# Optimization experiments

Measured on AMD Instinct MI355X. Metric: run time of the kernel, lower is better.

## Reference

```python
import jax, jax.numpy as jnp
import numpy as np

D_HEAD = 64

def setup_inputs() -> dict:
    key = jax.random.key(0)
    kq, kk, kv, kc = jax.random.split(key, 4)
    B, H, T, D = 2, 16, 2048, D_HEAD
    Q = jax.random.normal(kq, (B, H, T, D), dtype=jnp.float32)
    K = jax.random.normal(kk, (B, H, T, D), dtype=jnp.float32)
    V = jax.random.normal(kv, (B, H, T, D), dtype=jnp.float32)
    # causal mask: True = attend
    mask = jnp.tril(jnp.ones((T, T), dtype=jnp.bool_))
    curvature = jax.random.normal(kc, (H, D, D), dtype=jnp.float32) * 0.02
    return {"Q": Q, "K": K, "V": V, "mask": mask, "curvature": curvature}

def reference(Q, K, V, mask, curvature):
    scale = 1.0 / np.sqrt(Q.shape[-1]).astype(np.float32)
    # per-head learned rotation of Q
    Q_rot = jnp.einsum('bhtd,hde->bhte', Q, curvature)
    scores = jnp.einsum('bhtd,bhsd->bhts', Q_rot, K) * scale  # [B,H,T,T]
    scores = jnp.where(mask[None, None, :, :], scores, -jnp.inf)
    attn = jax.nn.softmax(scores, axis=-1)
    out = jnp.einsum('bhts,bhsd->bhtd', attn, V)
    return out
```

## Files before the change

kernel.cpp:

```cpp
#include <hip/hip_runtime.h>


typedef __attribute__((ext_vector_type(8))) short short8;
typedef __attribute__((ext_vector_type(8))) unsigned short ushort8;
typedef __attribute__((ext_vector_type(4))) float f32x4;
typedef __attribute__((ext_vector_type(2))) _Float16 half2v;
typedef __attribute__((ext_vector_type(4))) _Float16 half4;
typedef __attribute__((ext_vector_type(8))) _Float16 half8;

constexpr int Tc = 2048;
constexpr int Dc = 64;
constexpr size_t REGION = (size_t)32 * Tc * Dc;

__device__ inline unsigned short f2bf(float f) {
    union { float f; unsigned u; } x; x.f = f;
    return (unsigned short)((x.u + 0x7fffu + ((x.u >> 16) & 1u)) >> 16);
}

__device__ inline half2v pkrtz(float a, float b) {
    return __builtin_bit_cast(half2v, __builtin_amdgcn_cvt_pkrtz(a, b));
}

#define MFMA_BF16_K32(a, b, c) __builtin_amdgcn_mfma_f32_16x16x32_bf16((a), (b), (c), 0, 0, 0)
#define MFMA_F16_K16(a, b, c)  __builtin_amdgcn_mfma_f32_16x16x16f16((a), (b), (c), 0, 0, 0)

__global__ __launch_bounds__(256, 1)
void holo_cfrag(const float* __restrict__ Cp, unsigned short* __restrict__ cfrag_g)
{
    const int t = threadIdx.x, lane = t & 63, eb = t >> 6;
    const int l15 = lane & 15, quad = lane >> 4;
    const int h = blockIdx.x;
    const float* Cg = Cp + (size_t)h * Dc * Dc;
    #pragma unroll
    for (int half = 0; half < 2; ++half) {
        short8 b;
        #pragma unroll
        for (int jj = 0; jj < 8; ++jj) {
            const int d = half * 32 + quad * 8 + jj;
            b[jj] = (short)f2bf(Cg[d * Dc + eb * 16 + l15]);
        }
        *(short8*)(&cfrag_g[(((size_t)h * 4 + eb) * 2 + half) * 512 + lane * 8]) = b;
    }
}

__global__ __launch_bounds__(256, 4)
void holo_prep8(const float* __restrict__ Qp, const float* __restrict__ Kp,
                const float* __restrict__ Vp,
                const unsigned short* __restrict__ cfrag_g,
                unsigned short* __restrict__ qfrag_g,
                unsigned short* __restrict__ kfrag_g,
                _Float16* __restrict__ vfrag_g)
{
    __shared__ unsigned short kt[64 * 72];
    __shared__ unsigned short qt[64 * 72];
    __shared__ _Float16      vt[64 * 72];
    __shared__ unsigned short pf[64 * 72];

    const int t = threadIdx.x, lane = t & 63, w = t >> 6;
    const int l15 = lane & 15, quad = lane >> 4, wb = w * 16;
    const int n = blockIdx.x, bh = n >> 5, st = n & 31, h = bh & 15;
    const int s0 = st * 64;

    const float* Qg = Qp + ((size_t)bh * Tc + s0) * Dc;
    const float* Kg = Kp + ((size_t)bh * Tc + s0) * Dc;
    const float* Vg = Vp + ((size_t)bh * Tc + s0) * Dc;

    #pragma unroll
    for (int kk = 0; kk < 4; ++kk) {
        const int flat = kk * 1024 + t * 4;
        const int r = flat >> 6, d0 = flat & 63;
        float4 kv = *(const float4*)(&Kg[flat]);
        ushort4 kp; kp.x = f2bf(kv.x); kp.y = f2bf(kv.y); kp.z = f2bf(kv.z); kp.w = f2bf(kv.w);
        *(ushort4*)(&kt[r * 72 + d0]) = kp;
        float4 qv = *(const float4*)(&Qg[flat]);
        ushort4 qp; qp.x = f2bf(qv.x); qp.y = f2bf(qv.y); qp.z = f2bf(qv.z); qp.w = f2bf(qv.w);
        *(ushort4*)(&qt[r * 72 + d0]) = qp;
        float4 vv = *(const float4*)(&Vg[flat]);
        half4 vp;
        vp[0] = (_Float16)vv.x; vp[1] = (_Float16)vv.y;
        vp[2] = (_Float16)vv.z; vp[3] = (_Float16)vv.w;
        *(half4*)(&vt[r * 72 + d0]) = vp;
    }
    __syncthreads();

    {
        const int row = wb + l15;
        ushort8 p0 = *(const ushort8*)(&kt[row * 72 + quad * 8]);
        ushort8 p1 = *(const ushort8*)(&kt[row * 72 + 32 + quad * 8]);
        unsigned short* kdst = kfrag_g + (((size_t)(bh * 32 + st) * 4 + w) * 64 + lane) * 16;
        *(ushort8*)(kdst) = p0;
        *(ushort8*)(kdst + 8) = p1;
    }

    {
        half8 v0, v1;
        #pragma unroll
        for (int dn = 0; dn < 2; ++dn)
            #pragma unroll
            for (int i = 0; i < 4; ++i)
                v0[dn * 4 + i] = vt[(wb + quad * 4 + i) * 72 + dn * 16 + l15];
        #pragma unroll
        for (int dn = 0; dn < 2; ++dn)
            #pragma unroll
            for (int i = 0; i < 4; ++i)
                v1[dn * 4 + i] = vt[(wb + quad * 4 + i) * 72 + (dn + 2) * 16 + l15];
        _Float16* vdst = vfrag_g + (((size_t)(bh * 32 + st) * 4 + w) * 64 + lane) * 16;
        *(half8*)(vdst) = v0;
        *(half8*)(vdst + 8) = v1;
    }

    {
        short8 a0 = *(const short8*)(&qt[(wb + l15) * 72 + quad * 8]);
        short8 a1 = *(const short8*)(&qt[(wb + l15) * 72 + 32 + quad * 8]);
        #pragma unroll
        for (int eb = 0; eb < 4; ++eb) {
            short8 b0 = *(const short8*)(&cfrag_g[(((size_t)h * 4 + eb) * 2 + 0) * 512 + lane * 8]);
            short8 b1 = *(const short8*)(&cfrag_g[(((size_t)h * 4 + eb) * 2 + 1) * 512 + lane * 8]);
            f32x4 c = {0.f, 0.f, 0.f, 0.f};
            c = MFMA_BF16_K32(a0, b0, c);
            c = MFMA_BF16_K32(a1, b1, c);
            #pragma unroll
            for (int i = 0; i < 4; ++i)
                pf[(wb + quad * 4 + i) * 72 + eb * 16 + l15] = f2bf(c[i] * 0.18033688f);
        }
        __threadfence_block();
        short8 fa0 = *(const short8*)(&pf[(wb + l15) * 72 + quad * 8]);
        short8 fa1 = *(const short8*)(&pf[(wb + l15) * 72 + 32 + quad * 8]);
        const size_t strip = (size_t)bh * 128 + st * 4 + w;
        *(short8*)(&qfrag_g[strip * 1024 + lane * 8]) = fa0;
        *(short8*)(&qfrag_g[strip * 1024 + 512 + lane * 8]) = fa1;
    }
}

__global__ __launch_bounds__(256, 2)
void holo_attn10(const unsigned short* __restrict__ qfrag_g,
                 const unsigned short* __restrict__ kfrag_g,
                 const _Float16* __restrict__ vfrag_g,
                 float* __restrict__ Op)
{
    __shared__ float lds_o[2][2][16][68];
    __shared__ float lds_l[2][2][16];

    const int t = threadIdx.x, lane = t & 63, wid = t >> 6;
    const int l15 = lane & 15, quad = lane >> 4;
    const int hv  = wid & 1;
    const int par = wid >> 1;

    const int id = blockIdx.x;
    const int xcd = id & 7, sseq = id >> 3;
    const int qi = 31 - (sseq >> 2);
    const int bh = xcd * 4 + (sseq & 3);
    const int q0 = qi * 64;

    short8 qa0[2], qa1[2];
    #pragma unroll
    for (int s2 = 0; s2 < 2; ++s2) {
        const size_t strip = (size_t)bh * 128 + qi * 4 + (2 * hv + s2);
        qa0[s2] = *(const short8*)(&qfrag_g[strip * 1024 + lane * 8]);
        qa1[s2] = *(const short8*)(&qfrag_g[strip * 1024 + 512 + lane * 8]);
    }

    const unsigned short* kbase = kfrag_g + (size_t)bh * 32 * 4 * 1024;
    const _Float16*       vbase = vfrag_g + (size_t)bh * 32 * 4 * 1024;

    f32x4 o[2][4];
    #pragma unroll
    for (int s2 = 0; s2 < 2; ++s2)
        #pragma unroll
        for (int dn = 0; dn < 4; ++dn) o[s2][dn] = f32x4{0.f, 0.f, 0.f, 0.f};
    float l2[2] = {0.f, 0.f};

    const int rowgA = q0 + (2 * hv) * 16 + l15;
    const int rowgB = rowgA + 16;

    short8 kf0[4], kf1[4];
    half8 vlo[4], vhi[4];
    #pragma unroll
    for (int tn = 0; tn < 4; ++tn) {
        const unsigned short* kfb = kbase + (size_t)par * 4096 + ((size_t)tn * 64 + lane) * 16;
        kf0[tn] = *(const short8*)(kfb);
        kf1[tn] = *(const short8*)(kfb + 8);
        const _Float16* vfb = vbase + (size_t)par * 4096 + ((size_t)tn * 64 + lane) * 16;
        vlo[tn] = *(const half8*)(vfb);
        vhi[tn] = *(const half8*)(vfb + 8);
    }

    for (int j = par; j <= qi; j += 2) {
        f32x4 stA[4], stB[4];
        #pragma unroll
        for (int tn = 0; tn < 4; ++tn) {
            f32x4 cA = {0.f, 0.f, 0.f, 0.f};
            cA = MFMA_BF16_K32(kf0[tn], qa0[0], cA);
            cA = MFMA_BF16_K32(kf1[tn], qa1[0], cA);
            stA[tn] = cA;
            f32x4 cB = {0.f, 0.f, 0.f, 0.f};
            cB = MFMA_BF16_K32(kf0[tn], qa0[1], cB);
            cB = MFMA_BF16_K32(kf1[tn], qa1[1], cB);
            stB[tn] = cB;
        }

        const int jn = (j + 2 <= qi) ? j + 2 : j;
        #pragma unroll
        for (int tn = 0; tn < 4; ++tn) {
            const unsigned short* kfb = kbase + (size_t)jn * 4096 + ((size_t)tn * 64 + lane) * 16;
            kf0[tn] = *(const short8*)(kfb);
            kf1[tn] = *(const short8*)(kfb + 8);
        }

        half4 paA[4], paB[4];
        #pragma unroll
        for (int tn = 0; tn < 4; ++tn) {
            float pA[4], pB[4];
            #pragma unroll
            for (int i = 0; i < 4; ++i) {
                float svA = stA[tn][i], svB = stB[tn][i];
                if (j == qi) {
                    const int colg = j * 64 + tn * 16 + quad * 4 + i;
                    if (colg > rowgA) svA = -1e30f;
                    if (colg > rowgB) svB = -1e30f;
                }
                pA[i] = __builtin_amdgcn_exp2f(svA);
                pB[i] = __builtin_amdgcn_exp2f(svB);
                l2[0] += pA[i];
                l2[1] += pB[i];
            }
            half2v loA = pkrtz(pA[0], pA[1]), hiA = pkrtz(pA[2], pA[3]);
            paA[tn] = __builtin_shufflevector(loA, hiA, 0, 1, 2, 3);
            half2v loB = pkrtz(pB[0], pB[1]), hiB = pkrtz(pB[2], pB[3]);
            paB[tn] = __builtin_shufflevector(loB, hiB, 0, 1, 2, 3);
        }

        #pragma unroll
        for (int tn = 0; tn < 4; ++tn) {
            half4 vf0 = __builtin_shufflevector(vlo[tn], vlo[tn], 0, 1, 2, 3);
            half4 vf1 = __builtin_shufflevector(vlo[tn], vlo[tn], 4, 5, 6, 7);
            half4 vf2 = __builtin_shufflevector(vhi[tn], vhi[tn], 0, 1, 2, 3);
            half4 vf3 = __builtin_shufflevector(vhi[tn], vhi[tn], 4, 5, 6, 7);
            o[0][0] = MFMA_F16_K16(vf0, paA[tn], o[0][0]);
            o[0][1] = MFMA_F16_K16(vf1, paA[tn], o[0][1]);
            o[0][2] = MFMA_F16_K16(vf2, paA[tn], o[0][2]);
            o[0][3] = MFMA_F16_K16(vf3, paA[tn], o[0][3]);
            o[1][0] = MFMA_F16_K16(vf0, paB[tn], o[1][0]);
            o[1][1] = MFMA_F16_K16(vf1, paB[tn], o[1][1]);
            o[1][2] = MFMA_F16_K16(vf2, paB[tn], o[1][2]);
            o[1][3] = MFMA_F16_K16(vf3, paB[tn], o[1][3]);
        }

        #pragma unroll
        for (int tn = 0; tn < 4; ++tn) {
            const _Float16* vfb = vbase + (size_t)jn * 4096 + ((size_t)tn * 64 + lane) * 16;
            vlo[tn] = *(const half8*)(vfb);
            vhi[tn] = *(const half8*)(vfb + 8);
        }
    }

    #pragma unroll
    for (int s2 = 0; s2 < 2; ++s2) {
        l2[s2] += __shfl_xor(l2[s2], 16);
        l2[s2] += __shfl_xor(l2[s2], 32);
    }

    if (par == 1) {
        #pragma unroll
        for (int s2 = 0; s2 < 2; ++s2) {
            #pragma unroll
            for (int dn = 0; dn < 4; ++dn) {
                float4 r;
                r.x = o[s2][dn][0]; r.y = o[s2][dn][1];
                r.z = o[s2][dn][2]; r.w = o[s2][dn][3];
                *(float4*)(&lds_o[hv][s2][l15][dn * 16 + quad * 4]) = r;
            }
            if (quad == 0) lds_l[hv][s2][l15] = l2[s2];
        }
    }
    __syncthreads();
    if (par == 0) {
        #pragma unroll
        for (int s2 = 0; s2 < 2; ++s2) {
            const float inv = 1.0f / (l2[s2] + lds_l[hv][s2][l15]);
            const int rowg = q0 + (2 * hv + s2) * 16 + l15;
            float* dst = Op + ((size_t)bh * Tc + rowg) * Dc;
            const float* po = &lds_o[hv][s2][l15][0];
            #pragma unroll
            for (int dn = 0; dn < 4; ++dn) {
                float4 r;
                r.x = (o[s2][dn][0] + po[dn * 16 + quad * 4 + 0]) * inv;
                r.y = (o[s2][dn][1] + po[dn * 16 + quad * 4 + 1]) * inv;
                r.z = (o[s2][dn][2] + po[dn * 16 + quad * 4 + 2]) * inv;
                r.w = (o[s2][dn][3] + po[dn * 16 + quad * 4 + 3]) * inv;
                *(float4*)(&dst[dn * 16 + quad * 4]) = r;
            }
        }
    }
}

extern "C" void kernel_launch(void* const* d_in, const int* in_sizes, int n_in,
                              void* d_out, int out_size, void* d_ws, size_t ws_size,
                              hipStream_t stream) {
    const float* Q = (const float*)d_in[0];
    const float* K = (const float*)d_in[1];
    const float* V = (const float*)d_in[2];
    const float* C = (const float*)d_in[4];
    float* O = (float*)d_out;

    unsigned short* qfrag_w = (unsigned short*)d_ws;
    unsigned short* kfrag_w = qfrag_w + REGION;
    _Float16*       vfrag_w = (_Float16*)(kfrag_w + REGION);
    unsigned short* cfrag_w = (unsigned short*)(vfrag_w + REGION);

    holo_cfrag<<<dim3(16), dim3(256), 0, stream>>>(C, cfrag_w);
    holo_prep8<<<dim3(1024), dim3(256), 0, stream>>>(Q, K, V, cfrag_w, qfrag_w, kfrag_w, vfrag_w);
    holo_attn10<<<dim3(1024), dim3(256), 0, stream>>>(qfrag_w, kfrag_w, vfrag_w, O);
}
```

Before: 136.9 us.

## Split softmax-PV into two halves, add setprio around MFMA, raise occupancy to 3

The attention kernel's launch bounds go from 2 to 3 blocks per CU, which pushes the compiler toward lower register use and higher occupancy. The exp/pack/PV stage is split into two sequential halves (rows A then rows B) so fewer probability registers are live at once, and s_setprio raises wave priority during MFMA bursts so exp work from other waves can interleave. The next-tile loads are now skipped on the final iteration instead of reloading the current tile. The tighter register budget risks spills, and splitting the stage reduces instruction-level parallelism within a wave.

```diff
diff --git a/kernel.cpp b/kernel.cpp
--- a/kernel.cpp
+++ b/kernel.cpp
@@ -132,8 +132,8 @@
     }
 }
 
-__global__ __launch_bounds__(256, 2)
-void holo_attn10(const unsigned short* __restrict__ qfrag_g,
+__global__ __launch_bounds__(256, 3)
+void holo_attn11(const unsigned short* __restrict__ qfrag_g,
                  const unsigned short* __restrict__ kfrag_g,
                  const _Float16* __restrict__ vfrag_g,
                  float* __restrict__ Op)
@@ -186,71 +186,109 @@
     }
 
     for (int j = par; j <= qi; j += 2) {
+        const bool more = (j + 2 <= qi);
+        const int jn = j + 2;
+
         f32x4 stA[4], stB[4];
+        __builtin_amdgcn_s_setprio(1);
         #pragma unroll
         for (int tn = 0; tn < 4; ++tn) {
             f32x4 cA = {0.f, 0.f, 0.f, 0.f};
             cA = MFMA_BF16_K32(kf0[tn], qa0[0], cA);
             cA = MFMA_BF16_K32(kf1[tn], qa1[0], cA);
             stA[tn] = cA;
+        }
+        #pragma unroll
+        for (int tn = 0; tn < 4; ++tn) {
             f32x4 cB = {0.f, 0.f, 0.f, 0.f};
             cB = MFMA_BF16_K32(kf0[tn], qa0[1], cB);
             cB = MFMA_BF16_K32(kf1[tn], qa1[1], cB);
             stB[tn] = cB;
         }
-
-        const int jn = (j + 2 <= qi) ? j + 2 : j;
-        #pragma unroll
-        for (int tn = 0; tn < 4; ++tn) {
-            const unsigned short* kfb = kbase + (size_t)jn * 4096 + ((size_t)tn * 64 + lane) * 16;
-            kf0[tn] = *(const short8*)(kfb);
-            kf1[tn] = *(const short8*)(kfb + 8);
-        }
-
-        half4 paA[4], paB[4];
-        #pragma unroll
-        for (int tn = 0; tn < 4; ++tn) {
-            float pA[4], pB[4];
-            #pragma unroll
-            for (int i = 0; i < 4; ++i) {
-                float svA = stA[tn][i], svB = stB[tn][i];
-                if (j == qi) {
-                    const int colg = j * 64 + tn * 16 + quad * 4 + i;
-                    if (colg > rowgA) svA = -1e30f;
-                    if (colg > rowgB) svB = -1e30f;
+        __builtin_amdgcn_s_setprio(0);
+
+        if (more) {
+            #pragma unroll
+            for (int tn = 0; tn < 4; ++tn) {
+                const unsigned short* kfb = kbase + (size_t)jn * 4096 + ((size_t)tn * 64 + lane) * 16;
+                kf0[tn] = *(const short8*)(kfb);
+                kf1[tn] = *(const short8*)(kfb + 8);
+            }
+        }
+
+        {
+            half4 paA[4];
+            #pragma unroll
+            for (int tn = 0; tn < 4; ++tn) {
+                float p[4];
+                #pragma unroll
+                for (int i = 0; i < 4; ++i) {
+                    float sv = stA[tn][i];
+                    if (j == qi) {
+                        const int colg = j * 64 + tn * 16 + quad * 4 + i;
+                        if (colg > rowgA) sv = -1e30f;
+                    }
+                    p[i] = __builtin_amdgcn_exp2f(sv);
+                    l2[0] += p[i];
                 }
-                pA[i] = __builtin_amdgcn_exp2f(svA);
-                pB[i] = __builtin_amdgcn_exp2f(svB);
-                l2[0] += pA[i];
-                l2[1] += pB[i];
-            }
-            half2v loA = pkrtz(pA[0], pA[1]), hiA = pkrtz(pA[2], pA[3]);
-            paA[tn] = __builtin_shufflevector(loA, hiA, 0, 1, 2, 3);
-            half2v loB = pkrtz(pB[0], pB[1]), hiB = pkrtz(pB[2], pB[3]);
-            paB[tn] = __builtin_shufflevector(loB, hiB, 0, 1, 2, 3);
-        }
-
-        #pragma unroll
-        for (int tn = 0; tn < 4; ++tn) {
-            half4 vf0 = __builtin_shufflevector(vlo[tn], vlo[tn], 0, 1, 2, 3);
-            half4 vf1 = __builtin_shufflevector(vlo[tn], vlo[tn], 4, 5, 6, 7);
-            half4 vf2 = __builtin_shufflevector(vhi[tn], vhi[tn], 0, 1, 2, 3);
-            half4 vf3 = __builtin_shufflevector(vhi[tn], vhi[tn], 4, 5, 6, 7);
-            o[0][0] = MFMA_F16_K16(vf0, paA[tn], o[0][0]);
-            o[0][1] = MFMA_F16_K16(vf1, paA[tn], o[0][1]);
-            o[0][2] = MFMA_F16_K16(vf2, paA[tn], o[0][2]);
-            o[0][3] = MFMA_F16_K16(vf3, paA[tn], o[0][3]);
-            o[1][0] = MFMA_F16_K16(vf0, paB[tn], o[1][0]);
-            o[1][1] = MFMA_F16_K16(vf1, paB[tn], o[1][1]);
-            o[1][2] = MFMA_F16_K16(vf2, paB[tn], o[1][2]);
-            o[1][3] = MFMA_F16_K16(vf3, paB[tn], o[1][3]);
-        }
-
-        #pragma unroll
-        for (int tn = 0; tn < 4; ++tn) {
-            const _Float16* vfb = vbase + (size_t)jn * 4096 + ((size_t)tn * 64 + lane) * 16;
-            vlo[tn] = *(const half8*)(vfb);
-            vhi[tn] = *(const half8*)(vfb + 8);
+                half2v lo = pkrtz(p[0], p[1]), hi = pkrtz(p[2], p[3]);
+                paA[tn] = __builtin_shufflevector(lo, hi, 0, 1, 2, 3);
+            }
+            __builtin_amdgcn_s_setprio(1);
+            #pragma unroll
+            for (int tn = 0; tn < 4; ++tn) {
+                half4 vf0 = __builtin_shufflevector(vlo[tn], vlo[tn], 0, 1, 2, 3);
+                half4 vf1 = __builtin_shufflevector(vlo[tn], vlo[tn], 4, 5, 6, 7);
+                half4 vf2 = __builtin_shufflevector(vhi[tn], vhi[tn], 0, 1, 2, 3);
+                half4 vf3 = __builtin_shufflevector(vhi[tn], vhi[tn], 4, 5, 6, 7);
+                o[0][0] = MFMA_F16_K16(vf0, paA[tn], o[0][0]);
+                o[0][1] = MFMA_F16_K16(vf1, paA[tn], o[0][1]);
+                o[0][2] = MFMA_F16_K16(vf2, paA[tn], o[0][2]);
+                o[0][3] = MFMA_F16_K16(vf3, paA[tn], o[0][3]);
+            }
+            __builtin_amdgcn_s_setprio(0);
+        }
+
+        {
+            half4 paB[4];
+            #pragma unroll
+            for (int tn = 0; tn < 4; ++tn) {
+                float p[4];
+                #pragma unroll
+                for (int i = 0; i < 4; ++i) {
+                    float sv = stB[tn][i];
+                    if (j == qi) {
+                        const int colg = j * 64 + tn * 16 + quad * 4 + i;
+                        if (colg > rowgB) sv = -1e30f;
+                    }
+                    p[i] = __builtin_amdgcn_exp2f(sv);
+                    l2[1] += p[i];
+                }
+                half2v lo = pkrtz(p[0], p[1]), hi = pkrtz(p[2], p[3]);
+                paB[tn] = __builtin_shufflevector(lo, hi, 0, 1, 2, 3);
+            }
+            __builtin_amdgcn_s_setprio(1);
+            #pragma unroll
+            for (int tn = 0; tn < 4; ++tn) {
+                half4 vf0 = __builtin_shufflevector(vlo[tn], vlo[tn], 0, 1, 2, 3);
+                half4 vf1 = __builtin_shufflevector(vlo[tn], vlo[tn], 4, 5, 6, 7);
+                half4 vf2 = __builtin_shufflevector(vhi[tn], vhi[tn], 0, 1, 2, 3);
+                half4 vf3 = __builtin_shufflevector(vhi[tn], vhi[tn], 4, 5, 6, 7);
+                o[1][0] = MFMA_F16_K16(vf0, paB[tn], o[1][0]);
+                o[1][1] = MFMA_F16_K16(vf1, paB[tn], o[1][1]);
+                o[1][2] = MFMA_F16_K16(vf2, paB[tn], o[1][2]);
+                o[1][3] = MFMA_F16_K16(vf3, paB[tn], o[1][3]);
+            }
+            __builtin_amdgcn_s_setprio(0);
+        }
+
+        if (more) {
+            #pragma unroll
+            for (int tn = 0; tn < 4; ++tn) {
+                const _Float16* vfb = vbase + (size_t)jn * 4096 + ((size_t)tn * 64 + lane) * 16;
+                vlo[tn] = *(const half8*)(vfb);
+                vhi[tn] = *(const half8*)(vfb + 8);
+            }
         }
     }
 
@@ -310,5 +348,5 @@
 
     holo_cfrag<<<dim3(16), dim3(256), 0, stream>>>(C, cfrag_w);
     holo_prep8<<<dim3(1024), dim3(256), 0, stream>>>(Q, K, V, cfrag_w, qfrag_w, kfrag_w, vfrag_w);
-    holo_attn10<<<dim3(1024), dim3(256), 0, stream>>>(qfrag_w, kfrag_w, vfrag_w, O);
-}
+    holo_attn11<<<dim3(1024), dim3(256), 0, stream>>>(qfrag_w, kfrag_w, vfrag_w, O);
+}
```

Result: slower. 169.3 us (+23.7%).
